# Optimization experiments

Hardware: AMD Instinct MI355X
Metric: run time of the kernel (lower is better)

## Reference

```python
import jax, jax.numpy as jnp
import numpy as np

# --- module hyperparameters (init_kwargs) ---
K = 64
PZ, PY, PX = 5, 5, 5          # patch_size
PROJ = 512                     # projection_dim
B, C, D, H, W = 4, 256, 32, 64, 64


def setup_inputs() -> dict:
    key = jax.random.key(0)
    k1, k2, k3, k4 = jax.random.split(key, 4)
    feature_map = jax.random.normal(k1, (B, C, D, H, W), jnp.float32)
    score_map = jax.random.normal(k2, (B, 1, D, H, W), jnp.float32)
    # LazyLinear(projection_dim) materialized: in_features = C * K
    Wp = jax.random.normal(k3, (PROJ, C * K), jnp.float32) / np.sqrt(C * K).astype(np.float32)
    b = jax.random.normal(k4, (PROJ,), jnp.float32) * 0.01
    return {"feature_map": feature_map, "score_map": score_map, "Wp": Wp, "b": b}


def reference(feature_map, score_map, Wp, b):
    Bn, Cn, Dn, Hn, Wn = feature_map.shape
    flat = score_map.reshape(Bn, -1)                      # (B, D*H*W)
    scores, idx = jax.lax.top_k(flat, K)                  # (B, K)
    z = idx // (Hn * Wn)
    y = (idx % (Hn * Wn)) // Wn
    x = idx % Wn
    centers = jnp.stack([z, y, x], axis=-1)               # (B, K, 3)

    # boundary-clamped window origins: z0 = max(cz - dz//2, 0), window [z0, min(z0+dz, D))
    z0 = jnp.maximum(z - PZ // 2, 0)
    y0 = jnp.maximum(y - PY // 2, 0)
    x0 = jnp.maximum(x - PX // 2, 0)

    def per_batch(fm, z0b, y0b, x0b):
        # fm: (C, D, H, W); z0b/y0b/x0b: (K,)
        iz = z0b[:, None] + jnp.arange(PZ)                # (K, PZ)
        iy = y0b[:, None] + jnp.arange(PY)
        ix = x0b[:, None] + jnp.arange(PX)
        mz, my, mx = iz < Dn, iy < Hn, ix < Wn            # out-of-range => excluded from mean
        iz = jnp.minimum(iz, Dn - 1)
        iy = jnp.minimum(iy, Hn - 1)
        ix = jnp.minimum(ix, Wn - 1)
        # gather fixed-size patches: (C, K, PZ, PY, PX)
        patch = fm[:, iz[:, :, None, None], iy[:, None, :, None], ix[:, None, None, :]]
        mask = (mz[:, :, None, None] & my[:, None, :, None] & mx[:, None, None, :]).astype(fm.dtype)  # (K,PZ,PY,PX)
        s = jnp.einsum('ckzyx,kzyx->kc', patch, mask)     # masked sum -> (K, C)
        cnt = mask.sum(axis=(-3, -2, -1))                 # (K,) = actual clamped patch volume
        return (s / cnt[:, None]).reshape(-1)             # (K*C,) — patch-major, matching torch cat order

    vec = jax.vmap(per_batch)(feature_map, z0, y0, x0)    # (B, K*C)
    feature = vec @ Wp.T + b                              # (B, PROJ)
    return centers, scores, feature
```

## Files before the change

kernel.cpp:

```cpp
#include <hip/hip_runtime.h>
#include <hip/hip_bf16.h>

#define Bn   4
#define Cn   256
#define Dn   32
#define Hn   64
#define Wn   64
#define Kt   64
#define PROJ 512
#define DHW  (Dn*Hn*Wn)
#define HW   (Hn*Wn)
#define VECLEN (Kt*Cn)

#define NBIN    4096
#define CANDMAX 4096
#define SLOT    128
#define STATIC_THR 3.0f

#define WS_CAND_OFF 0
#define WS_IDX_OFF  (256*1024)
#define WS_VEC_OFF  (260*1024)

#define OUT_SCORES 768
#define OUT_FEAT   1024

__device__ __forceinline__ unsigned f2sortable(float f) {
    unsigned u = __float_as_uint(f);
    return (u & 0x80000000u) ? ~u : (u | 0x80000000u);
}
__device__ __forceinline__ float sortable2f(unsigned u) {
    unsigned orig = (u & 0x80000000u) ? (u & 0x7FFFFFFFu) : ~u;
    return __uint_as_float(orig);
}

__global__ __launch_bounds__(256) void compact_kernel(
        const float* __restrict__ score, unsigned long long* __restrict__ cand) {
    __shared__ unsigned long long lc[SLOT - 1];
    __shared__ int lcnt;
    const int blk = blockIdx.x;
    const int b   = blk >> 6;
    const int sub = blk & 63;
    const int tid = threadIdx.x;
    if (tid == 0) lcnt = 0;
    __syncthreads();

    const unsigned thr = f2sortable(STATIC_THR);
    const float4* src = (const float4*)(score + (size_t)b * DHW) + sub * 512;
    #pragma unroll
    for (int i = tid; i < 512; i += 256) {
        float4 v = src[i];
        unsigned gbase = (unsigned)((sub * 512 + i) * 4);
        float vals[4] = {v.x, v.y, v.z, v.w};
        #pragma unroll
        for (int l = 0; l < 4; ++l) {
            unsigned u = f2sortable(vals[l]);
            if (u >= thr) {
                int pos = atomicAdd(&lcnt, 1);
                if (pos < SLOT - 1)
                    lc[pos] = ((unsigned long long)u << 32) |
                              (0xFFFFFFFFu - (gbase + l));
            }
        }
    }
    __syncthreads();

    unsigned long long* cb = cand + (size_t)blk * SLOT;
    int n = lcnt;
    if (n > SLOT - 1) n = SLOT;
    if (tid == 0) cb[0] = (unsigned long long)n;
    int m = (n > SLOT - 1) ? (SLOT - 1) : n;
    for (int i = tid; i < m; i += 256) cb[1 + i] = lc[i];
}

__global__ __launch_bounds__(256) void final_kernel(
        const float* __restrict__ score,
        const unsigned long long* __restrict__ cand,
        float* __restrict__ out, int* __restrict__ sorted_idx) {
    __shared__ unsigned long long keys[CANDMAX];
    __shared__ unsigned long long win[Kt];
    __shared__ unsigned sgidx[Kt];
    __shared__ int lh[NBIN];
    __shared__ int partial[256];
    __shared__ int cnts[64], offs[64];
    __shared__ int s_n, s_thr, s_cnt, s_ovf;
    const int b   = blockIdx.x;
    const int tid = threadIdx.x;

    if (tid == 0) { s_ovf = 0; s_cnt = 0; }
    __syncthreads();
    if (tid < 64) {
        int c = (int)cand[(size_t)((b << 6) + tid) * SLOT];
        if (c > SLOT - 1) atomicOr(&s_ovf, 1);
        cnts[tid] = c;
    }
    __syncthreads();
    if (tid == 0) {
        int o = 0;
        for (int s = 0; s < 64; ++s) { offs[s] = o; o += cnts[s]; }
        s_n = o;
    }
    __syncthreads();

    int n = s_n;
    if (!s_ovf && n >= Kt && n <= CANDMAX) {
        for (int s = 0; s < 64; ++s) {
            int c = cnts[s], o = offs[s];
            const unsigned long long* cb =
                cand + (size_t)((b << 6) + s) * SLOT + 1;
            for (int i = tid; i < c; i += 256) keys[o + i] = cb[i];
        }
        __syncthreads();
    } else {
        for (int i = tid; i < NBIN; i += 256) lh[i] = 0;
        __syncthreads();
        const float4* src = (const float4*)(score + (size_t)b * DHW);
        for (int i = tid; i < DHW / 4; i += 256) {
            float4 v = src[i];
            atomicAdd(&lh[f2sortable(v.x) >> 20], 1);
            atomicAdd(&lh[f2sortable(v.y) >> 20], 1);
            atomicAdd(&lh[f2sortable(v.z) >> 20], 1);
            atomicAdd(&lh[f2sortable(v.w) >> 20], 1);
        }
        __syncthreads();
        {
            int base = NBIN - 16 - 16 * tid;
            int s = 0;
            #pragma unroll
            for (int i = 0; i < 16; ++i) s += lh[base + i];
            partial[tid] = s;
        }
        __syncthreads();
        if (tid == 0) {
            int cum = 0, T = 0;
            for (int j = 0; j < 256; ++j) {
                if (cum + partial[j] >= Kt) {
                    int bb = NBIN - 1 - 16 * j;
                    for (int i = 0; i < 16; ++i) {
                        cum += lh[bb - i];
                        if (cum >= Kt) { T = bb - i; break; }
                    }
                    break;
                }
                cum += partial[j];
            }
            s_thr = T;
        }
        __syncthreads();
        const unsigned thr = (unsigned)s_thr;
        for (int i = tid; i < DHW / 4; i += 256) {
            float4 v = src[i];
            float vals[4] = {v.x, v.y, v.z, v.w};
            #pragma unroll
            for (int l = 0; l < 4; ++l) {
                unsigned u = f2sortable(vals[l]);
                if ((u >> 20) >= thr) {
                    int pos = atomicAdd(&s_cnt, 1);
                    if (pos < CANDMAX)
                        keys[pos] = ((unsigned long long)u << 32) |
                                    (0xFFFFFFFFu - (unsigned)(4 * i + l));
                }
            }
        }
        __syncthreads();
        n = s_cnt;
        if (n > CANDMAX) n = CANDMAX;
    }

    for (int i = tid; i < n; i += 256) {
        unsigned long long k = keys[i];
        int r = 0;
        for (int j = 0; j < n; ++j) r += (keys[j] > k);
        if (r < Kt) win[r] = k;
    }
    __syncthreads();

    if (tid < Kt) {
        unsigned long long kk = win[tid];
        float sc = sortable2f((unsigned)(kk >> 32));
        unsigned gidx = 0xFFFFFFFFu - (unsigned)(kk & 0xFFFFFFFFu);
        int z = (int)(gidx >> 12);
        int y = (int)((gidx >> 6) & 63);
        int x = (int)(gidx & 63);
        int o = (b * Kt + tid) * 3;
        out[o + 0] = (float)z;
        out[o + 1] = (float)y;
        out[o + 2] = (float)x;
        out[OUT_SCORES + b * Kt + tid] = sc;
        sgidx[tid] = gidx;
    }
    __syncthreads();
    if (tid < Kt) {
        unsigned g = sgidx[tid];
        int r = 0;
        #pragma unroll
        for (int j = 0; j < Kt; ++j) r += (sgidx[j] < g);
        sorted_idx[b * Kt + r] = (int)((unsigned)(tid << 20) | g);
    }
}

__global__ __launch_bounds__(256) void gather_kernel(
        const float* __restrict__ fm, const int* __restrict__ sorted_idx,
        float* __restrict__ vec) {
    const int blk = blockIdx.x;
    const int b   = blk >> 6;
    const int cg  = blk & 63;
    const int tid = threadIdx.x;
    const int k   = tid & 63;
    const int c   = cg * 4 + (tid >> 6);

    const int e     = sorted_idx[b * Kt + k];
    const int idx   = e & 0xFFFFF;
    const int korig = ((unsigned)e) >> 20;
    const int z = idx >> 12;
    const int y = (idx >> 6) & 63;
    const int x = idx & 63;
    const int z0 = max(z - 2, 0), y0 = max(y - 2, 0), x0 = max(x - 2, 0);
    const int nz = min(5, Dn - z0), ny = min(5, Hn - y0), nx = min(5, Wn - x0);
    const int xe = x0 + nx;
    const int a0 = x0 & ~3;
    const bool need2 = (a0 + 4) < xe;

    float m[8];
    #pragma unroll
    for (int j = 0; j < 8; ++j) {
        int e2 = a0 + j;
        m[j] = (e2 >= x0 && e2 < xe) ? 1.f : 0.f;
    }

    const float* base = fm + ((size_t)(b * Cn + c)) * DHW
                           + (size_t)z0 * HW + (size_t)y0 * Wn;
    float s = 0.f;
    #pragma unroll
    for (int iz = 0; iz < 5; ++iz) {
        #pragma unroll
        for (int iy = 0; iy < 5; ++iy) {
            if (iz < nz && iy < ny) {
                const float* row = base + iz * HW + iy * Wn;
                float4 v0 = *(const float4*)(row + a0);
                s = fmaf(v0.x, m[0], s);
                s = fmaf(v0.y, m[1], s);
                s = fmaf(v0.z, m[2], s);
                s = fmaf(v0.w, m[3], s);
                if (need2) {
                    float4 v1 = *(const float4*)(row + a0 + 4);
                    s = fmaf(v1.x, m[4], s);
                    s = fmaf(v1.y, m[5], s);
                    s = fmaf(v1.z, m[6], s);
                    s = fmaf(v1.w, m[7], s);
                }
            }
        }
    }
    vec[((size_t)(b * Kt + korig) << 8) + c] = s / (float)(nz * ny * nx);
}

__global__ __launch_bounds__(256) void gemv_kernel(
        const float* __restrict__ vec, const float* __restrict__ Wp,
        const float* __restrict__ bias, float* __restrict__ out) {
    const int p   = blockIdx.x;
    const int tid = threadIdx.x;
    const float4* w4 = (const float4*)(Wp + (size_t)p * VECLEN);

    float acc[Bn] = {0.f, 0.f, 0.f, 0.f};
    for (int i = tid; i < VECLEN / 4; i += 256) {
        float4 wv = w4[i];
        #pragma unroll
        for (int bb = 0; bb < Bn; ++bb) {
            float4 vv = ((const float4*)(vec + bb * VECLEN))[i];
            acc[bb] += wv.x * vv.x + wv.y * vv.y + wv.z * vv.z + wv.w * vv.w;
        }
    }

    __shared__ float red[4][Bn];
    const int lane = tid & 63, wave = tid >> 6;
    #pragma unroll
    for (int bb = 0; bb < Bn; ++bb) {
        float v = acc[bb];
        #pragma unroll
        for (int off = 32; off > 0; off >>= 1) v += __shfl_down(v, off, 64);
        if (lane == 0) red[wave][bb] = v;
    }
    __syncthreads();
    if (tid < Bn) {
        int bb = tid;
        float t = red[0][bb] + red[1][bb] + red[2][bb] + red[3][bb];
        out[OUT_FEAT + bb * PROJ + p] = t + bias[p];
    }
}

extern "C" void kernel_launch(void* const* d_in, const int* in_sizes, int n_in,
                              void* d_out, int out_size, void* d_ws, size_t ws_size,
                              hipStream_t stream) {
    const float* fm    = (const float*)d_in[0];
    const float* score = (const float*)d_in[1];
    const float* Wp    = (const float*)d_in[2];
    const float* bias  = (const float*)d_in[3];
    float* out = (float*)d_out;

    char* ws = (char*)d_ws;
    unsigned long long* cand = (unsigned long long*)(ws + WS_CAND_OFF);
    int*   sorted_idx = (int*)(ws + WS_IDX_OFF);
    float* vec        = (float*)(ws + WS_VEC_OFF);

    compact_kernel<<<Bn * 64, 256, 0, stream>>>(score, cand);
    final_kernel<<<Bn, 256, 0, stream>>>(score, cand, out, sorted_idx);
    gather_kernel<<<Bn * 64, 256, 0, stream>>>(fm, sorted_idx, vec);
    gemv_kernel<<<PROJ, 256, 0, stream>>>(vec, Wp, bias, out);
}
```

Baseline: 65.54 us.

## Fuse top-k selection into gather kernel and compute two outputs per GEMV block

Removes the separate 4-block final_kernel. Each of the 256 gather blocks now redundantly rebuilds the per-batch top-64 from the compacted candidates in shared memory and then gathers its channel group directly, which saves one launch and the serial low-occupancy stage. Candidate packing now uses per-slot atomics instead of a serial prefix scan, so key order varies but the rank-based selection does not depend on it. The GEMV now handles two projection rows per block so each vec load is reused twice. The cost is 64x redundant selection work per batch and heavier shared memory per gather block.

```diff
diff --git a/kernel.cpp b/kernel.cpp
--- a/kernel.cpp
+++ b/kernel.cpp
@@ -18,7 +18,6 @@
 #define STATIC_THR 3.0f
 
 #define WS_CAND_OFF 0
-#define WS_IDX_OFF  (256*1024)
 #define WS_VEC_OFF  (260*1024)
 
 #define OUT_SCORES 768
@@ -72,46 +71,43 @@
     for (int i = tid; i < m; i += 256) cb[1 + i] = lc[i];
 }
 
-__global__ __launch_bounds__(256) void final_kernel(
-        const float* __restrict__ score,
+__global__ __launch_bounds__(256) void gather_kernel(
+        const float* __restrict__ fm, const float* __restrict__ score,
         const unsigned long long* __restrict__ cand,
-        float* __restrict__ out, int* __restrict__ sorted_idx) {
+        float* __restrict__ out, float* __restrict__ vec) {
     __shared__ unsigned long long keys[CANDMAX];
     __shared__ unsigned long long win[Kt];
     __shared__ unsigned sgidx[Kt];
+    __shared__ int ssorted[Kt];
     __shared__ int lh[NBIN];
     __shared__ int partial[256];
-    __shared__ int cnts[64], offs[64];
-    __shared__ int s_n, s_thr, s_cnt, s_ovf;
-    const int b   = blockIdx.x;
+    __shared__ int s_cnt, s_thr, s_ovf;
+    const int blk = blockIdx.x;
+    const int b   = blk >> 6;
+    const int cg  = blk & 63;
     const int tid = threadIdx.x;
 
-    if (tid == 0) { s_ovf = 0; s_cnt = 0; }
-    __syncthreads();
+    if (tid == 0) { s_cnt = 0; s_ovf = 0; }
+    __syncthreads();
+
     if (tid < 64) {
-        int c = (int)cand[(size_t)((b << 6) + tid) * SLOT];
-        if (c > SLOT - 1) atomicOr(&s_ovf, 1);
-        cnts[tid] = c;
-    }
-    __syncthreads();
-    if (tid == 0) {
-        int o = 0;
-        for (int s = 0; s < 64; ++s) { offs[s] = o; o += cnts[s]; }
-        s_n = o;
-    }
-    __syncthreads();
-
-    int n = s_n;
-    if (!s_ovf && n >= Kt && n <= CANDMAX) {
-        for (int s = 0; s < 64; ++s) {
-            int c = cnts[s], o = offs[s];
-            const unsigned long long* cb =
-                cand + (size_t)((b << 6) + s) * SLOT + 1;
-            for (int i = tid; i < c; i += 256) keys[o + i] = cb[i];
-        }
-        __syncthreads();
-    } else {
+        const unsigned long long* cb = cand + (size_t)((b << 6) + tid) * SLOT;
+        int c = (int)cb[0];
+        if (c > SLOT - 1) {
+            atomicOr(&s_ovf, 1);
+        } else if (c > 0) {
+            int o = atomicAdd(&s_cnt, c);
+            for (int i = 0; i < c; ++i)
+                if (o + i < CANDMAX) keys[o + i] = cb[1 + i];
+        }
+    }
+    __syncthreads();
+
+    int n = s_cnt;
+    if (s_ovf || n < Kt || n > CANDMAX) {
+        __syncthreads();
         for (int i = tid; i < NBIN; i += 256) lh[i] = 0;
+        if (tid == 0) s_cnt = 0;
         __syncthreads();
         const float4* src = (const float4*)(score + (size_t)b * DHW);
         for (int i = tid; i < DHW / 4; i += 256) {
@@ -176,17 +172,19 @@
 
     if (tid < Kt) {
         unsigned long long kk = win[tid];
-        float sc = sortable2f((unsigned)(kk >> 32));
         unsigned gidx = 0xFFFFFFFFu - (unsigned)(kk & 0xFFFFFFFFu);
-        int z = (int)(gidx >> 12);
-        int y = (int)((gidx >> 6) & 63);
-        int x = (int)(gidx & 63);
-        int o = (b * Kt + tid) * 3;
-        out[o + 0] = (float)z;
-        out[o + 1] = (float)y;
-        out[o + 2] = (float)x;
-        out[OUT_SCORES + b * Kt + tid] = sc;
         sgidx[tid] = gidx;
+        if (cg == 0) {
+            float sc = sortable2f((unsigned)(kk >> 32));
+            int z = (int)(gidx >> 12);
+            int y = (int)((gidx >> 6) & 63);
+            int x = (int)(gidx & 63);
+            int o = (b * Kt + tid) * 3;
+            out[o + 0] = (float)z;
+            out[o + 1] = (float)y;
+            out[o + 2] = (float)x;
+            out[OUT_SCORES + b * Kt + tid] = sc;
+        }
     }
     __syncthreads();
     if (tid < Kt) {
@@ -194,97 +192,99 @@
         int r = 0;
         #pragma unroll
         for (int j = 0; j < Kt; ++j) r += (sgidx[j] < g);
-        sorted_idx[b * Kt + r] = (int)((unsigned)(tid << 20) | g);
-    }
-}
-
-__global__ __launch_bounds__(256) void gather_kernel(
-        const float* __restrict__ fm, const int* __restrict__ sorted_idx,
-        float* __restrict__ vec) {
-    const int blk = blockIdx.x;
-    const int b   = blk >> 6;
-    const int cg  = blk & 63;
-    const int tid = threadIdx.x;
-    const int k   = tid & 63;
-    const int c   = cg * 4 + (tid >> 6);
-
-    const int e     = sorted_idx[b * Kt + k];
-    const int idx   = e & 0xFFFFF;
-    const int korig = ((unsigned)e) >> 20;
-    const int z = idx >> 12;
-    const int y = (idx >> 6) & 63;
-    const int x = idx & 63;
-    const int z0 = max(z - 2, 0), y0 = max(y - 2, 0), x0 = max(x - 2, 0);
-    const int nz = min(5, Dn - z0), ny = min(5, Hn - y0), nx = min(5, Wn - x0);
-    const int xe = x0 + nx;
-    const int a0 = x0 & ~3;
-    const bool need2 = (a0 + 4) < xe;
-
-    float m[8];
-    #pragma unroll
-    for (int j = 0; j < 8; ++j) {
-        int e2 = a0 + j;
-        m[j] = (e2 >= x0 && e2 < xe) ? 1.f : 0.f;
-    }
-
-    const float* base = fm + ((size_t)(b * Cn + c)) * DHW
-                           + (size_t)z0 * HW + (size_t)y0 * Wn;
-    float s = 0.f;
-    #pragma unroll
-    for (int iz = 0; iz < 5; ++iz) {
-        #pragma unroll
-        for (int iy = 0; iy < 5; ++iy) {
-            if (iz < nz && iy < ny) {
-                const float* row = base + iz * HW + iy * Wn;
-                float4 v0 = *(const float4*)(row + a0);
-                s = fmaf(v0.x, m[0], s);
-                s = fmaf(v0.y, m[1], s);
-                s = fmaf(v0.z, m[2], s);
-                s = fmaf(v0.w, m[3], s);
-                if (need2) {
-                    float4 v1 = *(const float4*)(row + a0 + 4);
-                    s = fmaf(v1.x, m[4], s);
-                    s = fmaf(v1.y, m[5], s);
-                    s = fmaf(v1.z, m[6], s);
-                    s = fmaf(v1.w, m[7], s);
+        ssorted[r] = (int)((unsigned)(tid << 20) | g);
+    }
+    __syncthreads();
+
+    {
+        const int k = tid & 63;
+        const int c = cg * 4 + (tid >> 6);
+
+        const int e     = ssorted[k];
+        const int idx   = e & 0xFFFFF;
+        const int korig = ((unsigned)e) >> 20;
+        const int z = idx >> 12;
+        const int y = (idx >> 6) & 63;
+        const int x = idx & 63;
+        const int z0 = max(z - 2, 0), y0 = max(y - 2, 0), x0 = max(x - 2, 0);
+        const int nz = min(5, Dn - z0), ny = min(5, Hn - y0), nx = min(5, Wn - x0);
+        const int xe = x0 + nx;
+        const int a0 = x0 & ~3;
+        const bool need2 = (a0 + 4) < xe;
+
+        float m[8];
+        #pragma unroll
+        for (int j = 0; j < 8; ++j) {
+            int e2 = a0 + j;
+            m[j] = (e2 >= x0 && e2 < xe) ? 1.f : 0.f;
+        }
+
+        const float* base = fm + ((size_t)(b * Cn + c)) * DHW
+                               + (size_t)z0 * HW + (size_t)y0 * Wn;
+        float s = 0.f;
+        #pragma unroll
+        for (int iz = 0; iz < 5; ++iz) {
+            #pragma unroll
+            for (int iy = 0; iy < 5; ++iy) {
+                if (iz < nz && iy < ny) {
+                    const float* row = base + iz * HW + iy * Wn;
+                    float4 v0 = *(const float4*)(row + a0);
+                    s = fmaf(v0.x, m[0], s);
+                    s = fmaf(v0.y, m[1], s);
+                    s = fmaf(v0.z, m[2], s);
+                    s = fmaf(v0.w, m[3], s);
+                    if (need2) {
+                        float4 v1 = *(const float4*)(row + a0 + 4);
+                        s = fmaf(v1.x, m[4], s);
+                        s = fmaf(v1.y, m[5], s);
+                        s = fmaf(v1.z, m[6], s);
+                        s = fmaf(v1.w, m[7], s);
+                    }
                 }
             }
         }
-    }
-    vec[((size_t)(b * Kt + korig) << 8) + c] = s / (float)(nz * ny * nx);
+        vec[((size_t)(b * Kt + korig) << 8) + c] = s / (float)(nz * ny * nx);
+    }
 }
 
 __global__ __launch_bounds__(256) void gemv_kernel(
         const float* __restrict__ vec, const float* __restrict__ Wp,
         const float* __restrict__ bias, float* __restrict__ out) {
-    const int p   = blockIdx.x;
+    __shared__ float gred[4][8];
+    const int p0  = blockIdx.x * 2;
     const int tid = threadIdx.x;
-    const float4* w4 = (const float4*)(Wp + (size_t)p * VECLEN);
-
-    float acc[Bn] = {0.f, 0.f, 0.f, 0.f};
+    const float4* w0 = (const float4*)(Wp + (size_t)p0 * VECLEN);
+    const float4* w1 = (const float4*)(Wp + (size_t)(p0 + 1) * VECLEN);
+
+    float acc0[Bn] = {0.f, 0.f, 0.f, 0.f};
+    float acc1[Bn] = {0.f, 0.f, 0.f, 0.f};
     for (int i = tid; i < VECLEN / 4; i += 256) {
-        float4 wv = w4[i];
+        float4 a = w0[i];
+        float4 c = w1[i];
         #pragma unroll
         for (int bb = 0; bb < Bn; ++bb) {
             float4 vv = ((const float4*)(vec + bb * VECLEN))[i];
-            acc[bb] += wv.x * vv.x + wv.y * vv.y + wv.z * vv.z + wv.w * vv.w;
-        }
-    }
-
-    __shared__ float red[4][Bn];
+            acc0[bb] += a.x * vv.x + a.y * vv.y + a.z * vv.z + a.w * vv.w;
+            acc1[bb] += c.x * vv.x + c.y * vv.y + c.z * vv.z + c.w * vv.w;
+        }
+    }
+
     const int lane = tid & 63, wave = tid >> 6;
     #pragma unroll
     for (int bb = 0; bb < Bn; ++bb) {
-        float v = acc[bb];
-        #pragma unroll
-        for (int off = 32; off > 0; off >>= 1) v += __shfl_down(v, off, 64);
-        if (lane == 0) red[wave][bb] = v;
-    }
-    __syncthreads();
-    if (tid < Bn) {
-        int bb = tid;
-        float t = red[0][bb] + red[1][bb] + red[2][bb] + red[3][bb];
-        out[OUT_FEAT + bb * PROJ + p] = t + bias[p];
+        float v0 = acc0[bb], v1 = acc1[bb];
+        #pragma unroll
+        for (int off = 32; off > 0; off >>= 1) {
+            v0 += __shfl_down(v0, off, 64);
+            v1 += __shfl_down(v1, off, 64);
+        }
+        if (lane == 0) { gred[wave][bb * 2] = v0; gred[wave][bb * 2 + 1] = v1; }
+    }
+    __syncthreads();
+    if (tid < 8) {
+        int bb = tid >> 1, q = tid & 1;
+        float t = gred[0][tid] + gred[1][tid] + gred[2][tid] + gred[3][tid];
+        out[OUT_FEAT + bb * PROJ + p0 + q] = t + bias[p0 + q];
     }
 }
 
@@ -299,11 +299,9 @@
 
     char* ws = (char*)d_ws;
     unsigned long long* cand = (unsigned long long*)(ws + WS_CAND_OFF);
-    int*   sorted_idx = (int*)(ws + WS_IDX_OFF);
-    float* vec        = (float*)(ws + WS_VEC_OFF);
+    float* vec = (float*)(ws + WS_VEC_OFF);
 
     compact_kernel<<<Bn * 64, 256, 0, stream>>>(score, cand);
-    final_kernel<<<Bn, 256, 0, stream>>>(score, cand, out, sorted_idx);
-    gather_kernel<<<Bn * 64, 256, 0, stream>>>(fm, sorted_idx, vec);
-    gemv_kernel<<<PROJ, 256, 0, stream>>>(vec, Wp, bias, out);
-}
+    gather_kernel<<<Bn * 64, 256, 0, stream>>>(fm, score, cand, out, vec);
+    gemv_kernel<<<PROJ / 2, 256, 0, stream>>>(vec, Wp, bias, out);
+}
```

Result: faster. 59.38 us (median of 2 runs) (-9.4%).
